# Kernel tuning notes

Measured on AMD Instinct MI355X. Metric: run time of the kernel, lower is better.

## Reference

```python
import jax, jax.numpy as jnp
import numpy as np

HEAD_SIZE = 64

def setup_inputs() -> dict:
    key = jax.random.key(0)
    k1, k2, k3, k4 = jax.random.split(key, 4)
    B, T, C = 4, 4096, 768
    s = 1.0 / np.sqrt(C)
    return {
        "x": jax.random.normal(k1, (B, T, C), dtype=jnp.float32),
        "Wq": jax.random.normal(k2, (C, HEAD_SIZE), dtype=jnp.float32) * s,
        "Wk": jax.random.normal(k3, (C, HEAD_SIZE), dtype=jnp.float32) * s,
        "Wv": jax.random.normal(k4, (C, HEAD_SIZE), dtype=jnp.float32) * s,
    }

def reference(x, Wq, Wk, Wv):
    # x: [B,T,C]; Wq/Wk/Wv: [C,H]
    T = x.shape[1]
    q = jnp.einsum('btc,ch->bth', x, Wq)
    k = jnp.einsum('btc,ch->bth', x, Wk)
    v = jnp.einsum('btc,ch->bth', x, Wv)
    scale = HEAD_SIZE ** (-0.5)
    wei = jnp.einsum('bth,bsh->bts', q, k) * scale  # [B,T,T]
    causal = jnp.tril(jnp.ones((T, T), dtype=bool))
    wei = jnp.where(causal, wei, -jnp.inf)
    wei = jax.nn.softmax(wei, axis=-1)
    # dropout p=0.0 -> identity
    out = jnp.einsum('bts,bsh->bth', wei, v)  # [B,T,H]
    return out
```

## Files before the change

kernel.cpp:

```cpp
#include <hip/hip_runtime.h>
#include <hip/hip_bf16.h>
#include <stdint.h>

typedef unsigned short u16;
typedef __attribute__((ext_vector_type(8))) __bf16 bf16x8;
typedef __attribute__((ext_vector_type(4))) float f32x4;

#define LOG2E 1.44269504088896340736f
#define FIXED_M 16.0f

__device__ inline u16 f2bf(float f){
  uint32_t u = __float_as_uint(f);
  u += 0x7FFFu + ((u >> 16) & 1u);
  return (u16)(u >> 16);
}
__device__ inline float bf2f(u16 v){
  return __uint_as_float(((uint32_t)v) << 16);
}

__global__ __launch_bounds__(256) void wt_kernel(const float* __restrict__ Wq,
                                                 const float* __restrict__ Wk,
                                                 const float* __restrict__ Wv,
                                                 u16* __restrict__ wtf){
  int idx = blockIdx.x * 256 + threadIdx.x;
  if (idx >= 192 * 768) return;
  int n = idx / 768, c = idx - n * 768;
  int h = n & 63;
  const float* W = (n < 64) ? Wq : ((n < 128) ? Wk : Wv);
  float v = W[c * 64 + h];
  if (n < 64) v *= 0.125f * LOG2E;
  int f = n >> 4, n16 = n & 15;
  int kstep = c >> 5, quad = (c >> 3) & 3, j = c & 7;
  wtf[(size_t)((f * 24 + kstep) * 64 + quad * 16 + n16) * 8 + j] = f2bf(v);
}

__global__ __launch_bounds__(256) void proj_kernel(const float* __restrict__ x,
                                                   const u16* __restrict__ wtf,
                                                   u16* __restrict__ qs,
                                                   u16* __restrict__ ks,
                                                   u16* __restrict__ vt){
  __shared__ float red[4][16][196];
  const int tid = threadIdx.x;
  const int w = tid >> 6, lane = tid & 63;
  const int n16 = lane & 15, quad = lane >> 4;
  const int rt = blockIdx.x * 16;
  const float* xr = x + (size_t)(rt + n16) * 768 + w * 192;

  const f32x4 fz = {0.f, 0.f, 0.f, 0.f};
  f32x4 acc[12];
#pragma unroll
  for (int f = 0; f < 12; ++f) acc[f] = fz;

#pragma unroll
  for (int kl = 0; kl < 6; ++kl){
    const float4 xa = *(const float4*)(xr + kl * 32 + quad * 8);
    const float4 xb = *(const float4*)(xr + kl * 32 + quad * 8 + 4);
    union { bf16x8 v; u16 e[8]; } ua;
    ua.e[0] = f2bf(xa.x); ua.e[1] = f2bf(xa.y);
    ua.e[2] = f2bf(xa.z); ua.e[3] = f2bf(xa.w);
    ua.e[4] = f2bf(xb.x); ua.e[5] = f2bf(xb.y);
    ua.e[6] = f2bf(xb.z); ua.e[7] = f2bf(xb.w);
#pragma unroll
    for (int f = 0; f < 12; ++f){
      bf16x8 bfrag = *(const bf16x8*)(wtf + (size_t)((f * 24 + w * 6 + kl) * 64 + lane) * 8);
      acc[f] = __builtin_amdgcn_mfma_f32_16x16x32_bf16(ua.v, bfrag, acc[f], 0, 0, 0);
    }
  }

#pragma unroll
  for (int f = 0; f < 12; ++f){
#pragma unroll
    for (int r = 0; r < 4; ++r)
      red[w][quad * 4 + r][f * 16 + n16] = acc[f][r];
  }
  __syncthreads();

  const int m = tid & 15, cg = tid >> 4;
  const int orow = rt + m;
  const int b = orow >> 12, t = orow & 4095;
#pragma unroll
  for (int i = 0; i < 12; ++i){
    int n = cg * 12 + i;
    float s = red[0][m][n] + red[1][m][n] + red[2][m][n] + red[3][m][n];
    u16 val = f2bf(s);
    if (n < 64)       qs[(size_t)orow * 64 + n]        = val;
    else if (n < 128) ks[(size_t)orow * 64 + (n - 64)] = val;
    else              vt[((size_t)b * 64 + (n - 128)) * 4096 + t] = val;
  }
}

__global__ __launch_bounds__(256) void flash_part(const u16* __restrict__ qs,
                                                  const u16* __restrict__ ks,
                                                  const u16* __restrict__ vtg,
                                                  u16* __restrict__ Opart,
                                                  float* __restrict__ ml){
  const int b  = blockIdx.x >> 8;
  const int qt = (blockIdx.x >> 2) & 63;
  const int ck = blockIdx.x & 3;
  const int kt0 = ck * 16;
  if (kt0 > qt) return;
  const int kt1 = min(qt, kt0 + 15);

  __shared__ u16 Ks[64 * 72];
  __shared__ u16 Vt[64 * 72];
  __shared__ u16 Ps[4 * 16 * 72];
  const int tid = threadIdx.x;
  const int w = tid >> 6, lane = tid & 63;
  const int n16 = lane & 15, quad = lane >> 4;
  const size_t bo = (size_t)b * 4096 * 64;
  const u16* qb = qs + bo;
  const u16* kb = ks + bo;
  const u16* vb = vtg + bo;

  const int qrow = qt * 64 + w * 16 + n16;
  bf16x8 qA0 = *(const bf16x8*)(qb + (size_t)qrow * 64 + quad * 8);
  bf16x8 qA1 = *(const bf16x8*)(qb + (size_t)qrow * 64 + 32 + quad * 8);

  const f32x4 fz = {0.f, 0.f, 0.f, 0.f};
  f32x4 O[4];
  float rs[4] = {0.f, 0.f, 0.f, 0.f};
#pragma unroll
  for (int f = 0; f < 4; ++f) O[f] = fz;

  const int c0r = tid >> 3,          c0p = tid & 7;
  const int c1r = (tid + 256) >> 3,  c1p = tid & 7;

  uint4 rk0 = *(const uint4*)(kb + (size_t)kt0 * 4096 + c0r * 64 + c0p * 8);
  uint4 rk1 = *(const uint4*)(kb + (size_t)kt0 * 4096 + c1r * 64 + c1p * 8);
  uint4 rv0 = *(const uint4*)(vb + (size_t)c0r * 4096 + kt0 * 64 + c0p * 8);
  uint4 rv1 = *(const uint4*)(vb + (size_t)c1r * 4096 + kt0 * 64 + c1p * 8);

  for (int kt = kt0; kt <= kt1; ++kt){
    *(uint4*)&Ks[c0r * 72 + c0p * 8] = rk0;
    *(uint4*)&Ks[c1r * 72 + c1p * 8] = rk1;
    *(uint4*)&Vt[c0r * 72 + c0p * 8] = rv0;
    *(uint4*)&Vt[c1r * 72 + c1p * 8] = rv1;
    __syncthreads();

    if (kt < kt1){
      rk0 = *(const uint4*)(kb + (size_t)(kt + 1) * 4096 + c0r * 64 + c0p * 8);
      rk1 = *(const uint4*)(kb + (size_t)(kt + 1) * 4096 + c1r * 64 + c1p * 8);
      rv0 = *(const uint4*)(vb + (size_t)c0r * 4096 + (kt + 1) * 64 + c0p * 8);
      rv1 = *(const uint4*)(vb + (size_t)c1r * 4096 + (kt + 1) * 64 + c1p * 8);
    }

    f32x4 S[4];
#pragma unroll
    for (int f = 0; f < 4; ++f){
      bf16x8 b0 = *(const bf16x8*)&Ks[(f * 16 + n16) * 72 + quad * 8];
      bf16x8 b1 = *(const bf16x8*)&Ks[(f * 16 + n16) * 72 + 32 + quad * 8];
      f32x4 s = fz;
      s = __builtin_amdgcn_mfma_f32_16x16x32_bf16(qA0, b0, s, 0, 0, 0);
      s = __builtin_amdgcn_mfma_f32_16x16x32_bf16(qA1, b1, s, 0, 0, 0);
      S[f] = s;
    }

    if (kt == qt){
#pragma unroll
      for (int f = 0; f < 4; ++f){
#pragma unroll
        for (int r = 0; r < 4; ++r){
          int col = kt * 64 + f * 16 + n16;
          int row = qt * 64 + w * 16 + quad * 4 + r;
          if (col > row) S[f][r] = -1e30f;
        }
      }
    }

#pragma unroll
    for (int f = 0; f < 4; ++f){
#pragma unroll
      for (int r = 0; r < 4; ++r){
        float p = __builtin_amdgcn_exp2f(S[f][r] - FIXED_M);
        S[f][r] = p;
        rs[r] += p;
      }
    }

#pragma unroll
    for (int f = 0; f < 4; ++f){
#pragma unroll
      for (int r = 0; r < 4; ++r)
        Ps[(w * 16 + quad * 4 + r) * 72 + f * 16 + n16] = f2bf(S[f][r]);
    }
    bf16x8 pA0 = *(const bf16x8*)&Ps[(w * 16 + n16) * 72 + quad * 8];
    bf16x8 pA1 = *(const bf16x8*)&Ps[(w * 16 + n16) * 72 + 32 + quad * 8];

#pragma unroll
    for (int f = 0; f < 4; ++f){
      bf16x8 v0 = *(const bf16x8*)&Vt[(f * 16 + n16) * 72 + quad * 8];
      bf16x8 v1 = *(const bf16x8*)&Vt[(f * 16 + n16) * 72 + 32 + quad * 8];
      O[f] = __builtin_amdgcn_mfma_f32_16x16x32_bf16(pA0, v0, O[f], 0, 0, 0);
      O[f] = __builtin_amdgcn_mfma_f32_16x16x32_bf16(pA1, v1, O[f], 0, 0, 0);
    }
    __syncthreads();
  }

#pragma unroll
  for (int r = 0; r < 4; ++r){
#pragma unroll
    for (int off = 1; off < 16; off <<= 1)
      rs[r] += __shfl_xor(rs[r], off, 16);
  }

  const size_t oidx = (size_t)blockIdx.x * 4096;
#pragma unroll
  for (int f = 0; f < 4; ++f){
#pragma unroll
    for (int r = 0; r < 4; ++r){
      int row_local = w * 16 + quad * 4 + r;
      Opart[oidx + (size_t)row_local * 64 + f * 16 + n16] = f2bf(O[f][r]);
    }
  }
  if (n16 == 0){
    float* lp = ml + (size_t)blockIdx.x * 64;
#pragma unroll
    for (int r = 0; r < 4; ++r)
      lp[w * 16 + quad * 4 + r] = rs[r];
  }
}

__global__ __launch_bounds__(256) void combine_kernel(const u16* __restrict__ Opart,
                                                      const float* __restrict__ ml,
                                                      float* __restrict__ out){
  const int bq = blockIdx.x;
  const int qt = bq & 63;
  const int nc = (qt >> 4) + 1;
  const int t = threadIdx.x;
  const int row = t >> 2, seg = t & 3;

  float L = 0.f;
  for (int c = 0; c < nc; ++c)
    L += ml[((size_t)bq * 4 + c) * 64 + row];
  const float invL = 1.0f / L;

  float acc[16];
#pragma unroll
  for (int j = 0; j < 16; ++j) acc[j] = 0.f;
  for (int c = 0; c < nc; ++c){
    const u16* p = Opart + ((size_t)bq * 4 + c) * 4096 + (size_t)row * 64 + seg * 16;
    uint4 d0 = *(const uint4*)p;
    uint4 d1 = *(const uint4*)(p + 8);
    const u16* e0 = (const u16*)&d0;
    const u16* e1 = (const u16*)&d1;
#pragma unroll
    for (int j = 0; j < 8; ++j){
      acc[j]     += bf2f(e0[j]);
      acc[8 + j] += bf2f(e1[j]);
    }
  }
  float* op = out + (size_t)bq * 4096 + (size_t)row * 64 + seg * 16;
#pragma unroll
  for (int j = 0; j < 4; ++j){
    float4 v = {acc[j*4] * invL, acc[j*4+1] * invL, acc[j*4+2] * invL, acc[j*4+3] * invL};
    *(float4*)(op + j * 4) = v;
  }
}

extern "C" void kernel_launch(void* const* d_in, const int* in_sizes, int n_in,
                              void* d_out, int out_size, void* d_ws, size_t ws_size,
                              hipStream_t stream){
  const float* x  = (const float*)d_in[0];
  const float* Wq = (const float*)d_in[1];
  const float* Wk = (const float*)d_in[2];
  const float* Wv = (const float*)d_in[3];
  float* out = (float*)d_out;

  u16* qs = (u16*)d_ws;
  u16* ks = qs + (size_t)16384 * 64;
  u16* vt = ks + (size_t)16384 * 64;
  u16* wtf = vt + (size_t)16384 * 64;
  u16* Opart = wtf + (size_t)192 * 768;
  float* ml = (float*)(Opart + (size_t)1024 * 4096);

  wt_kernel<<<576, 256, 0, stream>>>(Wq, Wk, Wv, wtf);
  proj_kernel<<<1024, 256, 0, stream>>>(x, wtf, qs, ks, vt);
  flash_part<<<1024, 256, 0, stream>>>(qs, ks, vt, Opart, ml);
  combine_kernel<<<256, 256, 0, stream>>>(Opart, ml, out);
}
```

Measured before the change: 150.2 us.

## Use 128-row query tiles with double-buffered K/V and reduction-free projection

The flash kernel now gives each wave 32 query rows instead of 16, so every K/V tile loaded into LDS is reused by twice as many rows. K/V tiles are double-buffered, which removes one barrier per iteration. The key range is split into 8 chunks of 8 tiles instead of 4 chunks of 16, and the combine kernel is remapped to match. The projection kernel drops its shared-memory split-K reduction: each wave computes the full 768-wide reduction for 48 output columns, launched as 512 blocks of 512 threads. The trade-off is more registers and LDS per block in the flash kernel, and more x reloads across waves in the projection.

```diff
diff --git a/kernel.cpp b/kernel.cpp
--- a/kernel.cpp
+++ b/kernel.cpp
@@ -34,58 +34,53 @@
   wtf[(size_t)((f * 24 + kstep) * 64 + quad * 16 + n16) * 8 + j] = f2bf(v);
 }
 
-__global__ __launch_bounds__(256) void proj_kernel(const float* __restrict__ x,
+__global__ __launch_bounds__(512) void proj_kernel(const float* __restrict__ x,
                                                    const u16* __restrict__ wtf,
                                                    u16* __restrict__ qs,
                                                    u16* __restrict__ ks,
                                                    u16* __restrict__ vt){
-  __shared__ float red[4][16][196];
   const int tid = threadIdx.x;
   const int w = tid >> 6, lane = tid & 63;
   const int n16 = lane & 15, quad = lane >> 4;
-  const int rt = blockIdx.x * 16;
-  const float* xr = x + (size_t)(rt + n16) * 768 + w * 192;
+  const int mt = w & 1, g = w >> 1;
+  const int rowbase = blockIdx.x * 32 + mt * 16;
+  const float* xr = x + (size_t)(rowbase + n16) * 768;
 
   const f32x4 fz = {0.f, 0.f, 0.f, 0.f};
-  f32x4 acc[12];
-#pragma unroll
-  for (int f = 0; f < 12; ++f) acc[f] = fz;
-
-#pragma unroll
-  for (int kl = 0; kl < 6; ++kl){
-    const float4 xa = *(const float4*)(xr + kl * 32 + quad * 8);
-    const float4 xb = *(const float4*)(xr + kl * 32 + quad * 8 + 4);
+  f32x4 acc[3];
+#pragma unroll
+  for (int i = 0; i < 3; ++i) acc[i] = fz;
+
+#pragma unroll
+  for (int kstep = 0; kstep < 24; ++kstep){
+    const float4 xa = *(const float4*)(xr + kstep * 32 + quad * 8);
+    const float4 xb = *(const float4*)(xr + kstep * 32 + quad * 8 + 4);
     union { bf16x8 v; u16 e[8]; } ua;
     ua.e[0] = f2bf(xa.x); ua.e[1] = f2bf(xa.y);
     ua.e[2] = f2bf(xa.z); ua.e[3] = f2bf(xa.w);
     ua.e[4] = f2bf(xb.x); ua.e[5] = f2bf(xb.y);
     ua.e[6] = f2bf(xb.z); ua.e[7] = f2bf(xb.w);
 #pragma unroll
-    for (int f = 0; f < 12; ++f){
-      bf16x8 bfrag = *(const bf16x8*)(wtf + (size_t)((f * 24 + w * 6 + kl) * 64 + lane) * 8);
-      acc[f] = __builtin_amdgcn_mfma_f32_16x16x32_bf16(ua.v, bfrag, acc[f], 0, 0, 0);
-    }
-  }
-
-#pragma unroll
-  for (int f = 0; f < 12; ++f){
-#pragma unroll
-    for (int r = 0; r < 4; ++r)
-      red[w][quad * 4 + r][f * 16 + n16] = acc[f][r];
-  }
-  __syncthreads();
-
-  const int m = tid & 15, cg = tid >> 4;
-  const int orow = rt + m;
-  const int b = orow >> 12, t = orow & 4095;
-#pragma unroll
-  for (int i = 0; i < 12; ++i){
-    int n = cg * 12 + i;
-    float s = red[0][m][n] + red[1][m][n] + red[2][m][n] + red[3][m][n];
-    u16 val = f2bf(s);
-    if (n < 64)       qs[(size_t)orow * 64 + n]        = val;
-    else if (n < 128) ks[(size_t)orow * 64 + (n - 64)] = val;
-    else              vt[((size_t)b * 64 + (n - 128)) * 4096 + t] = val;
+    for (int i = 0; i < 3; ++i){
+      bf16x8 bfrag = *(const bf16x8*)(wtf + (size_t)(((g * 3 + i) * 24 + kstep) * 64 + lane) * 8);
+      acc[i] = __builtin_amdgcn_mfma_f32_16x16x32_bf16(ua.v, bfrag, acc[i], 0, 0, 0);
+    }
+  }
+
+#pragma unroll
+  for (int i = 0; i < 3; ++i){
+    int n = g * 48 + i * 16 + n16;
+#pragma unroll
+    for (int r = 0; r < 4; ++r){
+      int orow = rowbase + quad * 4 + r;
+      u16 val = f2bf(acc[i][r]);
+      if (n < 64)       qs[(size_t)orow * 64 + n]        = val;
+      else if (n < 128) ks[(size_t)orow * 64 + (n - 64)] = val;
+      else {
+        int bb = orow >> 12, t = orow & 4095;
+        vt[((size_t)bb * 64 + (n - 128)) * 4096 + t] = val;
+      }
+    }
   }
 }
 
@@ -95,15 +90,16 @@
                                                   u16* __restrict__ Opart,
                                                   float* __restrict__ ml){
   const int b  = blockIdx.x >> 8;
-  const int qt = (blockIdx.x >> 2) & 63;
-  const int ck = blockIdx.x & 3;
-  const int kt0 = ck * 16;
-  if (kt0 > qt) return;
-  const int kt1 = min(qt, kt0 + 15);
-
-  __shared__ u16 Ks[64 * 72];
-  __shared__ u16 Vt[64 * 72];
-  __shared__ u16 Ps[4 * 16 * 72];
+  const int qt = (blockIdx.x >> 3) & 31;
+  const int ck = blockIdx.x & 7;
+  const int kt0 = ck * 8;
+  const int ktmax = 2 * qt + 1;
+  if (kt0 > ktmax) return;
+  const int kt1 = min(ktmax, kt0 + 7);
+
+  __shared__ u16 Ks[2][64 * 72];
+  __shared__ u16 Vt[2][64 * 72];
+  __shared__ u16 Ps[128 * 72];
   const int tid = threadIdx.x;
   const int w = tid >> 6, lane = tid & 63;
   const int n16 = lane & 15, quad = lane >> 4;
@@ -112,133 +108,171 @@
   const u16* kb = ks + bo;
   const u16* vb = vtg + bo;
 
-  const int qrow = qt * 64 + w * 16 + n16;
-  bf16x8 qA0 = *(const bf16x8*)(qb + (size_t)qrow * 64 + quad * 8);
-  bf16x8 qA1 = *(const bf16x8*)(qb + (size_t)qrow * 64 + 32 + quad * 8);
+  bf16x8 qA[2][2];
+#pragma unroll
+  for (int m = 0; m < 2; ++m){
+    const int qrow = qt * 128 + w * 32 + m * 16 + n16;
+    qA[m][0] = *(const bf16x8*)(qb + (size_t)qrow * 64 + quad * 8);
+    qA[m][1] = *(const bf16x8*)(qb + (size_t)qrow * 64 + 32 + quad * 8);
+  }
 
   const f32x4 fz = {0.f, 0.f, 0.f, 0.f};
-  f32x4 O[4];
-  float rs[4] = {0.f, 0.f, 0.f, 0.f};
-#pragma unroll
-  for (int f = 0; f < 4; ++f) O[f] = fz;
-
-  const int c0r = tid >> 3,          c0p = tid & 7;
-  const int c1r = (tid + 256) >> 3,  c1p = tid & 7;
+  f32x4 O[2][4];
+  float rs[2][4];
+#pragma unroll
+  for (int m = 0; m < 2; ++m)
+#pragma unroll
+    for (int f = 0; f < 4; ++f){ O[m][f] = fz; rs[m][f] = 0.f; }
+
+  const int c0r = tid >> 3, c0p = tid & 7;
+  const int c1r = c0r + 32;
 
   uint4 rk0 = *(const uint4*)(kb + (size_t)kt0 * 4096 + c0r * 64 + c0p * 8);
-  uint4 rk1 = *(const uint4*)(kb + (size_t)kt0 * 4096 + c1r * 64 + c1p * 8);
+  uint4 rk1 = *(const uint4*)(kb + (size_t)kt0 * 4096 + c1r * 64 + c0p * 8);
   uint4 rv0 = *(const uint4*)(vb + (size_t)c0r * 4096 + kt0 * 64 + c0p * 8);
-  uint4 rv1 = *(const uint4*)(vb + (size_t)c1r * 4096 + kt0 * 64 + c1p * 8);
-
+  uint4 rv1 = *(const uint4*)(vb + (size_t)c1r * 4096 + kt0 * 64 + c0p * 8);
+  *(uint4*)&Ks[0][c0r * 72 + c0p * 8] = rk0;
+  *(uint4*)&Ks[0][c1r * 72 + c0p * 8] = rk1;
+  *(uint4*)&Vt[0][c0r * 72 + c0p * 8] = rv0;
+  *(uint4*)&Vt[0][c1r * 72 + c0p * 8] = rv1;
+  if (kt0 < kt1){
+    rk0 = *(const uint4*)(kb + (size_t)(kt0 + 1) * 4096 + c0r * 64 + c0p * 8);
+    rk1 = *(const uint4*)(kb + (size_t)(kt0 + 1) * 4096 + c1r * 64 + c0p * 8);
+    rv0 = *(const uint4*)(vb + (size_t)c0r * 4096 + (kt0 + 1) * 64 + c0p * 8);
+    rv1 = *(const uint4*)(vb + (size_t)c1r * 4096 + (kt0 + 1) * 64 + c0p * 8);
+  }
+  __syncthreads();
+
+  int cur = 0;
   for (int kt = kt0; kt <= kt1; ++kt){
-    *(uint4*)&Ks[c0r * 72 + c0p * 8] = rk0;
-    *(uint4*)&Ks[c1r * 72 + c1p * 8] = rk1;
-    *(uint4*)&Vt[c0r * 72 + c0p * 8] = rv0;
-    *(uint4*)&Vt[c1r * 72 + c1p * 8] = rv1;
-    __syncthreads();
-
     if (kt < kt1){
-      rk0 = *(const uint4*)(kb + (size_t)(kt + 1) * 4096 + c0r * 64 + c0p * 8);
-      rk1 = *(const uint4*)(kb + (size_t)(kt + 1) * 4096 + c1r * 64 + c1p * 8);
-      rv0 = *(const uint4*)(vb + (size_t)c0r * 4096 + (kt + 1) * 64 + c0p * 8);
-      rv1 = *(const uint4*)(vb + (size_t)c1r * 4096 + (kt + 1) * 64 + c1p * 8);
-    }
-
-    f32x4 S[4];
+      const int nxt = cur ^ 1;
+      *(uint4*)&Ks[nxt][c0r * 72 + c0p * 8] = rk0;
+      *(uint4*)&Ks[nxt][c1r * 72 + c0p * 8] = rk1;
+      *(uint4*)&Vt[nxt][c0r * 72 + c0p * 8] = rv0;
+      *(uint4*)&Vt[nxt][c1r * 72 + c0p * 8] = rv1;
+      if (kt + 1 < kt1){
+        rk0 = *(const uint4*)(kb + (size_t)(kt + 2) * 4096 + c0r * 64 + c0p * 8);
+        rk1 = *(const uint4*)(kb + (size_t)(kt + 2) * 4096 + c1r * 64 + c0p * 8);
+        rv0 = *(const uint4*)(vb + (size_t)c0r * 4096 + (kt + 2) * 64 + c0p * 8);
+        rv1 = *(const uint4*)(vb + (size_t)c1r * 4096 + (kt + 2) * 64 + c0p * 8);
+      }
+    }
+
+    f32x4 S0[4], S1[4];
 #pragma unroll
     for (int f = 0; f < 4; ++f){
-      bf16x8 b0 = *(const bf16x8*)&Ks[(f * 16 + n16) * 72 + quad * 8];
-      bf16x8 b1 = *(const bf16x8*)&Ks[(f * 16 + n16) * 72 + 32 + quad * 8];
+      bf16x8 b0 = *(const bf16x8*)&Ks[cur][(f * 16 + n16) * 72 + quad * 8];
+      bf16x8 b1 = *(const bf16x8*)&Ks[cur][(f * 16 + n16) * 72 + 32 + quad * 8];
       f32x4 s = fz;
-      s = __builtin_amdgcn_mfma_f32_16x16x32_bf16(qA0, b0, s, 0, 0, 0);
-      s = __builtin_amdgcn_mfma_f32_16x16x32_bf16(qA1, b1, s, 0, 0, 0);
-      S[f] = s;
-    }
-
-    if (kt == qt){
+      s = __builtin_amdgcn_mfma_f32_16x16x32_bf16(qA[0][0], b0, s, 0, 0, 0);
+      s = __builtin_amdgcn_mfma_f32_16x16x32_bf16(qA[0][1], b1, s, 0, 0, 0);
+      S0[f] = s;
+      s = fz;
+      s = __builtin_amdgcn_mfma_f32_16x16x32_bf16(qA[1][0], b0, s, 0, 0, 0);
+      s = __builtin_amdgcn_mfma_f32_16x16x32_bf16(qA[1][1], b1, s, 0, 0, 0);
+      S1[f] = s;
+    }
+
+    if (kt >= 2 * qt){
 #pragma unroll
       for (int f = 0; f < 4; ++f){
 #pragma unroll
         for (int r = 0; r < 4; ++r){
           int col = kt * 64 + f * 16 + n16;
-          int row = qt * 64 + w * 16 + quad * 4 + r;
-          if (col > row) S[f][r] = -1e30f;
+          int row0 = qt * 128 + w * 32 + quad * 4 + r;
+          if (col > row0)      S0[f][r] = -1e30f;
+          if (col > row0 + 16) S1[f][r] = -1e30f;
         }
       }
     }
 
 #pragma unroll
+    for (int m = 0; m < 2; ++m){
+      f32x4* S = (m == 0) ? S0 : S1;
+#pragma unroll
+      for (int f = 0; f < 4; ++f){
+#pragma unroll
+        for (int r = 0; r < 4; ++r){
+          float p = __builtin_amdgcn_exp2f(S[f][r] - FIXED_M);
+          rs[m][r] += p;
+          Ps[(w * 32 + m * 16 + quad * 4 + r) * 72 + f * 16 + n16] = f2bf(p);
+        }
+      }
+    }
+    bf16x8 pA[2][2];
+#pragma unroll
+    for (int m = 0; m < 2; ++m){
+      pA[m][0] = *(const bf16x8*)&Ps[(w * 32 + m * 16 + n16) * 72 + quad * 8];
+      pA[m][1] = *(const bf16x8*)&Ps[(w * 32 + m * 16 + n16) * 72 + 32 + quad * 8];
+    }
+
+#pragma unroll
     for (int f = 0; f < 4; ++f){
+      bf16x8 v0 = *(const bf16x8*)&Vt[cur][(f * 16 + n16) * 72 + quad * 8];
+      bf16x8 v1 = *(const bf16x8*)&Vt[cur][(f * 16 + n16) * 72 + 32 + quad * 8];
+      O[0][f] = __builtin_amdgcn_mfma_f32_16x16x32_bf16(pA[0][0], v0, O[0][f], 0, 0, 0);
+      O[0][f] = __builtin_amdgcn_mfma_f32_16x16x32_bf16(pA[0][1], v1, O[0][f], 0, 0, 0);
+      O[1][f] = __builtin_amdgcn_mfma_f32_16x16x32_bf16(pA[1][0], v0, O[1][f], 0, 0, 0);
+      O[1][f] = __builtin_amdgcn_mfma_f32_16x16x32_bf16(pA[1][1], v1, O[1][f], 0, 0, 0);
+    }
+    __syncthreads();
+    cur ^= 1;
+  }
+
+#pragma unroll
+  for (int m = 0; m < 2; ++m)
+#pragma unroll
+    for (int r = 0; r < 4; ++r)
+#pragma unroll
+      for (int off = 1; off < 16; off <<= 1)
+        rs[m][r] += __shfl_xor(rs[m][r], off, 16);
+
+  const size_t oidx = (size_t)blockIdx.x * 8192;
+#pragma unroll
+  for (int m = 0; m < 2; ++m){
+#pragma unroll
+    for (int f = 0; f < 4; ++f){
 #pragma unroll
       for (int r = 0; r < 4; ++r){
-        float p = __builtin_amdgcn_exp2f(S[f][r] - FIXED_M);
-        S[f][r] = p;
-        rs[r] += p;
-      }
-    }
-
-#pragma unroll
-    for (int f = 0; f < 4; ++f){
+        int row_local = w * 32 + m * 16 + quad * 4 + r;
+        Opart[oidx + (size_t)row_local * 64 + f * 16 + n16] = f2bf(O[m][f][r]);
+      }
+    }
+  }
+  if (n16 == 0){
+    float* lp = ml + (size_t)blockIdx.x * 128;
+#pragma unroll
+    for (int m = 0; m < 2; ++m)
 #pragma unroll
       for (int r = 0; r < 4; ++r)
-        Ps[(w * 16 + quad * 4 + r) * 72 + f * 16 + n16] = f2bf(S[f][r]);
-    }
-    bf16x8 pA0 = *(const bf16x8*)&Ps[(w * 16 + n16) * 72 + quad * 8];
-    bf16x8 pA1 = *(const bf16x8*)&Ps[(w * 16 + n16) * 72 + 32 + quad * 8];
-
-#pragma unroll
-    for (int f = 0; f < 4; ++f){
-      bf16x8 v0 = *(const bf16x8*)&Vt[(f * 16 + n16) * 72 + quad * 8];
-      bf16x8 v1 = *(const bf16x8*)&Vt[(f * 16 + n16) * 72 + 32 + quad * 8];
-      O[f] = __builtin_amdgcn_mfma_f32_16x16x32_bf16(pA0, v0, O[f], 0, 0, 0);
-      O[f] = __builtin_amdgcn_mfma_f32_16x16x32_bf16(pA1, v1, O[f], 0, 0, 0);
-    }
-    __syncthreads();
-  }
-
-#pragma unroll
-  for (int r = 0; r < 4; ++r){
-#pragma unroll
-    for (int off = 1; off < 16; off <<= 1)
-      rs[r] += __shfl_xor(rs[r], off, 16);
-  }
-
-  const size_t oidx = (size_t)blockIdx.x * 4096;
-#pragma unroll
-  for (int f = 0; f < 4; ++f){
-#pragma unroll
-    for (int r = 0; r < 4; ++r){
-      int row_local = w * 16 + quad * 4 + r;
-      Opart[oidx + (size_t)row_local * 64 + f * 16 + n16] = f2bf(O[f][r]);
-    }
-  }
-  if (n16 == 0){
-    float* lp = ml + (size_t)blockIdx.x * 64;
-#pragma unroll
-    for (int r = 0; r < 4; ++r)
-      lp[w * 16 + quad * 4 + r] = rs[r];
+        lp[w * 32 + m * 16 + quad * 4 + r] = rs[m][r];
   }
 }
 
 __global__ __launch_bounds__(256) void combine_kernel(const u16* __restrict__ Opart,
                                                       const float* __restrict__ ml,
                                                       float* __restrict__ out){
-  const int bq = blockIdx.x;
-  const int qt = bq & 63;
-  const int nc = (qt >> 4) + 1;
+  const int blk = blockIdx.x;
+  const int half = blk & 1;
+  const int qtb = blk >> 1;
+  const int qt = qtb & 31;
+  const int b = qtb >> 5;
+  const int nc = ((2 * qt + 1) >> 3) + 1;
   const int t = threadIdx.x;
   const int row = t >> 2, seg = t & 3;
+  const int row_local = half * 64 + row;
 
   float L = 0.f;
   for (int c = 0; c < nc; ++c)
-    L += ml[((size_t)bq * 4 + c) * 64 + row];
+    L += ml[((size_t)qtb * 8 + c) * 128 + row_local];
   const float invL = 1.0f / L;
 
   float acc[16];
 #pragma unroll
   for (int j = 0; j < 16; ++j) acc[j] = 0.f;
   for (int c = 0; c < nc; ++c){
-    const u16* p = Opart + ((size_t)bq * 4 + c) * 4096 + (size_t)row * 64 + seg * 16;
+    const u16* p = Opart + ((size_t)qtb * 8 + c) * 8192 + (size_t)row_local * 64 + seg * 16;
     uint4 d0 = *(const uint4*)p;
     uint4 d1 = *(const uint4*)(p + 8);
     const u16* e0 = (const u16*)&d0;
@@ -249,7 +283,7 @@
       acc[8 + j] += bf2f(e1[j]);
     }
   }
-  float* op = out + (size_t)bq * 4096 + (size_t)row * 64 + seg * 16;
+  float* op = out + ((size_t)b * 4096 + qt * 128 + row_local) * 64 + seg * 16;
 #pragma unroll
   for (int j = 0; j < 4; ++j){
     float4 v = {acc[j*4] * invL, acc[j*4+1] * invL, acc[j*4+2] * invL, acc[j*4+3] * invL};
@@ -271,10 +305,10 @@
   u16* vt = ks + (size_t)16384 * 64;
   u16* wtf = vt + (size_t)16384 * 64;
   u16* Opart = wtf + (size_t)192 * 768;
-  float* ml = (float*)(Opart + (size_t)1024 * 4096);
+  float* ml = (float*)(Opart + (size_t)1024 * 8192);
 
   wt_kernel<<<576, 256, 0, stream>>>(Wq, Wk, Wv, wtf);
-  proj_kernel<<<1024, 256, 0, stream>>>(x, wtf, qs, ks, vt);
+  proj_kernel<<<512, 512, 0, stream>>>(x, wtf, qs, ks, vt);
   flash_part<<<1024, 256, 0, stream>>>(qs, ks, vt, Opart, ml);
   combine_kernel<<<256, 256, 0, stream>>>(Opart, ml, out);
 }
```

Measured after the change: 163.3 us. 1.09x slower.
